# Optimization experiments

Measured on AMD Instinct MI355X. Metric: run time of the kernel, lower is better.

## Reference

```python
import jax, jax.numpy as jnp
import numpy as np
from jax import lax

V_JOINTS = 25
N_SCALES = 13
C1 = 96
N_SEG = 50
EPS = 1e-5

# NTU RGB+D 25-joint skeleton edges (0-indexed)
_EDGES = [(0,1),(1,20),(2,20),(3,2),(4,20),(5,4),(6,5),(7,6),(8,20),(9,8),
          (10,9),(11,10),(12,0),(13,12),(14,13),(15,14),(16,0),(17,16),
          (18,17),(19,18),(21,22),(22,7),(23,24),(24,11)]


def _build_A_powers():
    # MS-G3D disentangled multi-scale adjacency: k-hop shells, D^-1/2 A D^-1/2 normalized
    A = np.zeros((V_JOINTS, V_JOINTS), dtype=np.float64)
    for i, j in _EDGES:
        A[i, j] = 1.0
        A[j, i] = 1.0
    I = np.eye(V_JOINTS)
    mats = []
    for k in range(N_SCALES):
        if k == 0:
            Ak = I.copy()
        else:
            Ak = (np.minimum(np.linalg.matrix_power(A + I, k), 1)
                  - np.minimum(np.linalg.matrix_power(A + I, k - 1), 1))
            Ak = Ak + I  # with_self=True
        d = Ak.sum(-1)
        Dinv = np.diag(d ** -0.5)
        mats.append(Dinv @ Ak @ Dinv)
    return np.concatenate(mats, axis=0).astype(np.float32)  # (13*25, 25)


def _segments(T, n_seg):
    # Segment boundaries exactly as the torch code: int(round(linspace(1, T, n_seg+1)))
    t_vec = [int(round(v)) for v in np.linspace(1, T, n_seg + 1)]
    lens = [t_vec[i + 1] - t_vec[i] for i in range(n_seg)]
    L = max(lens)
    idx = np.zeros((n_seg, L), dtype=np.int32)
    mask = np.zeros((n_seg, L), dtype=np.float32)
    for s in range(n_seg):
        start = t_vec[s] - 1
        for l in range(L):
            idx[s, l] = min(start + l, T - 2)
            mask[s, l] = 1.0 if l < lens[s] else 0.0
    sp_idx = np.array([t - 1 for t in t_vec[:-1]], dtype=np.int32)
    return idx, mask, sp_idx


def setup_inputs() -> dict:
    key = jax.random.key(0)
    ks = jax.random.split(key, 18)
    N, M, C, T, V = 4, 2, 3, 300, V_JOINTS
    num_classes = 60
    Cbn = M * C * V                       # 150
    Dlog = C1 + C1 * (C1 - 1) // 2        # 4656 (depth-2 logsig dims)
    Din = C1 + Dlog                       # 4752 (start pos + logsig)
    f = lambda k, s: jax.random.normal(k, s, dtype=jnp.float32)
    return {
        'x': f(ks[0], (N, M, C, T, V)),
        'bn_g': 1.0 + 0.1 * f(ks[1], (Cbn,)),
        'bn_b': 0.1 * f(ks[2], (Cbn,)),
        'bn_m': 0.1 * f(ks[3], (Cbn,)),
        'bn_v': jax.random.uniform(ks[4], (Cbn,), minval=0.5, maxval=1.5),
        'A_powers': jnp.asarray(_build_A_powers()),
        'A_res': jax.random.uniform(ks[5], (N_SCALES * V, V), minval=-1e-6, maxval=1e-6),
        'W_gcn': f(ks[6], (C1, N_SCALES * C)) / np.sqrt(N_SCALES * C),
        'b_gcn': 0.1 * f(ks[7], (C1,)),
        'bn2_g': 1.0 + 0.1 * f(ks[8], (C1,)),
        'bn2_b': 0.1 * f(ks[9], (C1,)),
        'bn2_m': 0.1 * f(ks[10], (C1,)),
        'bn2_v': jax.random.uniform(ks[11], (C1,), minval=0.5, maxval=1.5),
        'W_ih': f(ks[12], (4 * C1, Din)) / np.sqrt(Din),
        'W_hh': f(ks[13], (4 * C1, C1)) / np.sqrt(C1),
        'b_ih': 0.1 * f(ks[14], (4 * C1,)),
        'b_hh': 0.1 * f(ks[15], (4 * C1,)),
        'W_fc': f(ks[16], (num_classes, C1)) / np.sqrt(C1),
        'b_fc': 0.1 * f(ks[17], (num_classes,)),
    }


def reference(x, bn_g, bn_b, bn_m, bn_v, A_powers, A_res, W_gcn, b_gcn,
              bn2_g, bn2_b, bn2_m, bn2_v, W_ih, W_hh, b_ih, b_hh, W_fc, b_fc):
    N, M, C, T, V = x.shape
    NM = N * M
    # --- data_bn (inference BatchNorm1d over M*V*C channels) ---
    xb = x.transpose(0, 1, 4, 2, 3).reshape(N, M * V * C, T)
    xb = (xb - bn_m[:, None]) * (bn_g / jnp.sqrt(bn_v + EPS))[:, None] + bn_b[:, None]
    xg = xb.reshape(NM, V, C, T).transpose(0, 2, 3, 1)          # (NM, C, T, V)
    # --- MS_GCN: multi-scale disentangled graph conv ---
    A = A_powers + A_res                                        # (S*V, V)
    sup = jnp.einsum('vu,nctu->nctv', A, xg)                    # (NM, C, T, S*V)
    sup = sup.reshape(NM, C, T, N_SCALES, V).transpose(0, 3, 1, 2, 4)
    sup = sup.reshape(NM, N_SCALES * C, T, V)
    y = jnp.einsum('oc,nctv->notv', W_gcn, sup) + b_gcn[None, :, None, None]
    y = (y - bn2_m[None, :, None, None]) * (bn2_g / jnp.sqrt(bn2_v + EPS))[None, :, None, None] \
        + bn2_b[None, :, None, None]
    y = jax.nn.relu(y)                                          # (NM, C1, T, V)
    # --- LogSigRNN: per-joint temporal path, depth-2 log-signature per segment ---
    p = y.transpose(0, 3, 2, 1).reshape(NM * V, T, C1)          # (B, T, C1)
    idx, mask, sp_idx = _segments(T, N_SEG)
    dx = jnp.diff(p, axis=1)                                    # (B, T-1, C1)
    dseg = dx[:, idx] * mask[None, :, :, None]                  # (B, nseg, L, C1)
    pseg = jnp.cumsum(dseg, axis=2) - dseg                      # exclusive prefix within segment
    s1 = dseg.sum(axis=2)                                       # level-1: total increment
    Q = jnp.einsum('bslc,bsld->bscd', pseg, dseg)               # (B, nseg, C1, C1)
    levy = 0.5 * (Q - jnp.swapaxes(Q, -1, -2))                  # level-2 (Levy area)
    iu, ju = np.triu_indices(C1, 1)
    ls2 = levy[:, :, iu, ju]                                    # (B, nseg, 4560)
    start_pos = p[:, sp_idx, :]                                 # (B, nseg, C1)
    feat = jnp.concatenate([start_pos, s1, ls2], axis=-1)       # (B, nseg, 4752)
    # --- LSTM (torch gate order i,f,g,o) ---
    B = feat.shape[0]
    xw = jnp.einsum('btd,gd->btg', feat, W_ih) + (b_ih + b_hh)
    def step(carry, xt):
        h, c = carry
        g = xt + h @ W_hh.T
        i, fg, gg, o = jnp.split(g, 4, axis=-1)
        c = jax.nn.sigmoid(fg) * c + jax.nn.sigmoid(i) * jnp.tanh(gg)
        h = jax.nn.sigmoid(o) * jnp.tanh(c)
        return (h, c), h
    h0 = jnp.zeros((B, C1), feat.dtype)
    _, hs = lax.scan(step, (h0, h0), jnp.swapaxes(xw, 0, 1))
    hs = jnp.swapaxes(hs, 0, 1)                                 # (B, nseg, C1)
    out = hs.reshape(NM, V, N_SEG, C1).transpose(0, 3, 2, 1)    # (NM, C1, nseg, V)
    out = out.reshape(N, M, C1, -1).mean(axis=3).mean(axis=1)   # (N, C1)
    return out @ W_fc.T + b_fc
```

## Files before the change

kernel.cpp:

```cpp
#include <hip/hip_runtime.h>
#include <math.h>

#define KF 4752
#define KP 4768
#define KSTEPS 149
#define G4 384
#define NPAIR 4560
#define EPSBN 1e-5f
#define XWHALF 3840000

typedef float f32x4 __attribute__((ext_vector_type(4)));
typedef short s16x8 __attribute__((ext_vector_type(8)));

__device__ __forceinline__ unsigned short f2bf(float x){
  unsigned u = __float_as_uint(x);
  return (unsigned short)((u + 0x7fffu + ((u>>16)&1u)) >> 16);
}
__device__ __forceinline__ float bf2f(unsigned short h){
  return __uint_as_float(((unsigned)h)<<16);
}

__device__ __forceinline__ int seg_start(int s){ return (s<=24)? 6*s : 149 + 6*(s-25); }
__device__ __forceinline__ int seg_len(int s){ return (s==24)?5:6; }

#define NB_GEFF 1407
#define NB_BEFF 1200
#define NB_WSPL 7152

__global__ __launch_bounds__(256) void kPre(
    const float* bn_g,const float* bn_b,const float* bn_m,const float* bn_v,
    const float* Ap,const float* Ar,const float* Wg,const float* bg,
    const float* bn2_g,const float* bn2_b,const float* bn2_m,const float* bn2_v,
    const float* wih,
    float* geffT, float* beffT, unsigned short* whi, unsigned short* wlo)
{
  int bid = blockIdx.x, tid = threadIdx.x;
  if (bid < NB_GEFF){
    int idx = bid*256 + tid;
    if (idx >= 2*96*25*75) return;
    int cu = idx % 75; int rest = idx/75;
    int v = rest % 25; rest /= 25;
    int o = rest % 96; int m = rest / 96;
    int c = cu/25, u = cu%25;
    int ch = (m*25+u)*3 + c;
    float s1 = bn_g[ch] / sqrtf(bn_v[ch] + EPSBN);
    float s2 = bn2_g[o] / sqrtf(bn2_v[o] + EPSBN);
    float acc = 0.f;
    for (int k=0;k<13;k++){
      float a = Ap[(k*25+v)*25+u] + Ar[(k*25+v)*25+u];
      acc += Wg[o*39 + k*3 + c] * a;
    }
    geffT[((size_t)(m*75+cu))*2400 + v*96 + o] = acc * s1 * s2;
  } else if (bid < NB_GEFF + NB_BEFF){
    int wid  = ((bid-NB_GEFF)*256 + tid) >> 6;
    int lane = tid & 63;
    if (wid >= 2*96*25) return;
    int v = wid % 25; int rest = wid/25; int o = rest % 96; int m = rest/96;
    float acc = 0.f;
    #pragma unroll
    for (int it=0; it<16; ++it){
      int item = it*64 + lane;
      if (item < 975){
        int k = item / 75; int cu = item % 75; int c = cu/25, u = cu%25;
        int ch = (m*25+u)*3 + c;
        float s1 = bn_g[ch] / sqrtf(bn_v[ch] + EPSBN);
        float t1 = bn_b[ch] - bn_m[ch]*s1;
        float a  = Ap[(k*25+v)*25+u] + Ar[(k*25+v)*25+u];
        acc += Wg[o*39 + k*3 + c] * a * t1;
      }
    }
    #pragma unroll
    for (int off=32; off; off>>=1) acc += __shfl_down(acc, off);
    if (lane == 0){
      acc += bg[o];
      float s2 = bn2_g[o]/sqrtf(bn2_v[o]+EPSBN);
      beffT[m*2400 + v*96 + o] = s2*(acc - bn2_m[o]) + bn2_b[o];
    }
  } else {
    int idx = (bid - NB_GEFF - NB_BEFF)*256 + tid;
    if (idx >= G4*KP) return;
    int g = idx / KP, k = idx % KP;
    float v = (k < KF) ? wih[(size_t)g*KF + k] : 0.f;
    unsigned short h = f2bf(v);
    whi[idx] = h;
    wlo[idx] = f2bf(v - bf2f(h));
  }
}

#define TTILE 10
__global__ __launch_bounds__(256) void kP(const float* x, const float* geffT, const float* beffT, float* p){
  int nm = blockIdx.y;
  int t0 = blockIdx.x * TTILE;
  int m  = nm % 2;
  __shared__ float xs[75*TTILE];
  int tid = threadIdx.x;
  for (int li = tid; li < 75*TTILE; li += 256){
    int u = li % 25; int rest = li/25; int tt = rest % TTILE; int c = rest / TTILE;
    xs[(c*25+u)*TTILE + tt] = x[(((size_t)nm*3 + c)*300 + (t0+tt))*25 + u];
  }
  __syncthreads();
  const float* gT = geffT + (size_t)m*75*2400;
  for (int ow = tid; ow < 2400; ow += 256){
    int o = ow % 96, v = ow / 96;
    float b = beffT[m*2400 + ow];
    float acc[TTILE];
    #pragma unroll
    for (int t=0;t<TTILE;t++) acc[t] = b;
    for (int cu=0; cu<75; cu++){
      float gv = gT[(size_t)cu*2400 + ow];
      #pragma unroll
      for (int t=0;t<TTILE;t++) acc[t] += gv * xs[cu*TTILE+t];
    }
    #pragma unroll
    for (int t=0;t<TTILE;t++)
      p[((size_t)(nm*25+v)*300 + t0+t)*96 + o] = fmaxf(acc[t], 0.f);
  }
}

__global__ __launch_bounds__(256) void kFeat(const float* p,
                                             unsigned short* fhi, unsigned short* flo, int row0){
  int row = row0 + blockIdx.x;
  int b = row / 50, s = row % 50;
  int S = seg_start(s), len = seg_len(s);
  __shared__ float psL[6][96];
  __shared__ float dsL[6][96];
  __shared__ float qbuf[NPAIR];
  int tid = threadIdx.x;
  size_t base = (size_t)blockIdx.x * KP;
  if (tid < 96){
    int c = tid;
    float pv[7];
    #pragma unroll
    for (int l=0;l<7;l++) pv[l] = p[((size_t)b*300 + S + l)*96 + c];
    float run = 0.f;
    #pragma unroll
    for (int l=0;l<6;l++){
      float d = (l < len) ? (pv[l+1]-pv[l]) : 0.f;
      psL[l][c] = run; dsL[l][c] = d; run += d;
    }
    unsigned short h0 = f2bf(pv[0]);
    fhi[base + c] = h0; flo[base + c] = f2bf(pv[0] - bf2f(h0));
    unsigned short h1 = f2bf(run);
    fhi[base + 96 + c] = h1; flo[base + 96 + c] = f2bf(run - bf2f(h1));
  } else if (tid < 112){
    int c = KF + (tid - 96);
    fhi[base + c] = 0; flo[base + c] = 0;
  }
  __syncthreads();
  int ti = tid >> 4, tj = tid & 15;
  if (ti <= tj){
    int i0 = ti*6, j0 = tj*6;
    float q[6][6];
    #pragma unroll
    for (int a=0;a<6;a++)
      #pragma unroll
      for (int e=0;e<6;e++) q[a][e] = 0.f;
    #pragma unroll
    for (int l=0;l<6;l++){
      float pi[6], di[6], pj[6], dj[6];
      #pragma unroll
      for (int a=0;a<6;a++){
        pi[a] = psL[l][i0+a]; di[a] = dsL[l][i0+a];
        pj[a] = psL[l][j0+a]; dj[a] = dsL[l][j0+a];
      }
      #pragma unroll
      for (int a=0;a<6;a++)
        #pragma unroll
        for (int e=0;e<6;e++)
          q[a][e] += pi[a]*dj[e] - pj[e]*di[a];
    }
    #pragma unroll
    for (int a=0;a<6;a++){
      int i = i0 + a;
      int kb = i*95 - (i*(i-1))/2 - i - 1;
      #pragma unroll
      for (int e=0;e<6;e++){
        int j = j0 + e;
        if (j > i) qbuf[kb + j] = 0.5f*q[a][e];
      }
    }
  }
  __syncthreads();
  for (int g8 = tid; g8 < NPAIR/8; g8 += 256){
    f32x4 q0 = *(const f32x4*)&qbuf[g8*8];
    f32x4 q1 = *(const f32x4*)&qbuf[g8*8+4];
    float qa[8] = {q0.x,q0.y,q0.z,q0.w,q1.x,q1.y,q1.z,q1.w};
    s16x8 vh, vl;
    #pragma unroll
    for (int e=0;e<8;e++){
      unsigned short h = f2bf(qa[e]);
      vh[e] = (short)h;
      vl[e] = (short)f2bf(qa[e] - bf2f(h));
    }
    *(s16x8*)(fhi + base + 192 + g8*8) = vh;
    *(s16x8*)(flo + base + 192 + g8*8) = vl;
  }
}

__device__ __forceinline__ void gload16(const void* g, void* l){
  __builtin_amdgcn_global_load_lds(
      (const __attribute__((address_space(1))) void*)g,
      (__attribute__((address_space(3))) void*)l, 16, 0, 0);
}

__global__ __launch_bounds__(256) void kGemm(
    const unsigned short* __restrict__ fhi, const unsigned short* __restrict__ flo,
    const unsigned short* __restrict__ whi, const unsigned short* __restrict__ wlo,
    float* __restrict__ xw, int chunkRow0, int nrows)
{
  __shared__ unsigned short lds[20480];
  int tid  = threadIdx.x;
  int lane = tid & 63, w = tid >> 6;
  int id = blockIdx.x;
  int col = id & 1, zz = (id >> 1) & 3, mblk = id >> 3;
  int rowBase = mblk*128, colBase = col*192;
  int zbase = (zz==0) ? 0 : (38 + 37*(zz-1));
  int zSteps = (zz==0) ? 38 : 37;

  const unsigned short* gptr[10];
  int ldsOff[10];
  #pragma unroll
  for (int q=0;q<10;q++){
    int c = (w*10 + q)*64 + lane;
    const unsigned short* bp; int rr;
    if (c < 512)        { rr = c;        bp = fhi + (size_t)(rowBase + (rr>>2))*KP; }
    else if (c < 1024)  { rr = c-512;    bp = flo + (size_t)(rowBase + (rr>>2))*KP; }
    else if (c < 1792)  { rr = c-1024;   bp = whi + (size_t)(colBase + (rr>>2))*KP; }
    else                { rr = c-1792;   bp = wlo + (size_t)(colBase + (rr>>2))*KP; }
    int rw = rr>>2, gl = rr&3;
    int gs = gl ^ ((rw>>1)&3);
    gptr[q]  = bp + gs*8;
    ldsOff[q] = (w*10 + q)*512;
  }

  int wm = w & 1, wn = w >> 1;
  int gsel = lane >> 4, li = lane & 15;
  int aoff[4], boff[6];
  #pragma unroll
  for (int fm=0; fm<4; fm++){
    int r = wm*64 + fm*16 + li;
    aoff[fm] = r*32 + ((gsel ^ ((r>>1)&3))*8);
  }
  #pragma unroll
  for (int fn=0; fn<6; fn++){
    int r = wn*96 + fn*16 + li;
    boff[fn] = 8192 + r*32 + ((gsel ^ ((r>>1)&3))*8);
  }

  f32x4 acc[4][6];
  #pragma unroll
  for (int fm=0;fm<4;fm++)
    #pragma unroll
    for (int fn=0;fn<6;fn++) acc[fm][fn] = (f32x4){0.f,0.f,0.f,0.f};

  for (int t=0; t<zSteps; ++t){
    size_t ko = (size_t)(zbase + t)*32;
    #pragma unroll
    for (int q=0;q<10;q++) gload16(gptr[q] + ko, &lds[ldsOff[q]]);
    asm volatile("s_waitcnt vmcnt(0)" ::: "memory");
    __builtin_amdgcn_s_barrier();
    s16x8 bh[6], bl[6];
    #pragma unroll
    for (int fn=0;fn<6;fn++){
      bh[fn] = *(const s16x8*)(lds + boff[fn]);
      bl[fn] = *(const s16x8*)(lds + boff[fn] + 6144);
    }
    #pragma unroll
    for (int fm=0;fm<4;fm++){
      s16x8 ah = *(const s16x8*)(lds + aoff[fm]);
      s16x8 al = *(const s16x8*)(lds + aoff[fm] + 4096);
      #pragma unroll
      for (int fn=0;fn<6;fn++){
        acc[fm][fn] = __builtin_amdgcn_mfma_f32_16x16x32_bf16(ah, bh[fn], acc[fm][fn], 0,0,0);
        acc[fm][fn] = __builtin_amdgcn_mfma_f32_16x16x32_bf16(ah, bl[fn], acc[fm][fn], 0,0,0);
        acc[fm][fn] = __builtin_amdgcn_mfma_f32_16x16x32_bf16(al, bh[fn], acc[fm][fn], 0,0,0);
      }
    }
    __builtin_amdgcn_s_barrier();
  }

  int rl = (lane>>4)*4, cl = lane&15;
  float* outp = xw + (size_t)zz*XWHALF;
  #pragma unroll
  for (int fm=0;fm<4;fm++){
    #pragma unroll
    for (int fn=0;fn<6;fn++){
      int gr0 = rowBase + wm*64 + fm*16 + rl;
      int gc  = colBase + wn*96 + fn*16 + cl;
      f32x4 v = acc[fm][fn];
      #pragma unroll
      for (int r=0;r<4;r++){
        int gr = gr0 + r;
        if (gr < nrows)
          outp[(size_t)(chunkRow0 + gr)*G4 + gc] = v[r];
      }
    }
  }
}

__global__ __launch_bounds__(192) void kLstm(const float* xw, const float* whh,
                                             const float* bih, const float* bhh, float* hsum){
  int b = blockIdx.x;
  int t = threadIdx.x;
  int gA = t;
  int gB = t + 192;
  __shared__ __align__(16) float h_s[96];
  __shared__ float gbuf[384];
  float wA[96], wB[96];
  #pragma unroll
  for (int k=0;k<96;k++){ wA[k] = whh[(size_t)gA*96 + k]; wB[k] = whh[(size_t)gB*96 + k]; }
  float bA = bih[gA] + bhh[gA];
  float bB = bih[gB] + bhh[gB];
  float cval = 0.f, hacc = 0.f;
  if (t < 96) h_s[t] = 0.f;
  __syncthreads();
  const float* xr = xw + (size_t)b*50*G4;
  for (int st=0; st<50; st++){
    int o = st*G4;
    float aA = xr[o+gA] + xr[XWHALF+o+gA] + xr[2*(size_t)XWHALF+o+gA]
             + xr[3*(size_t)XWHALF+o+gA] + bA;
    float aB = xr[o+gB] + xr[XWHALF+o+gB] + xr[2*(size_t)XWHALF+o+gB]
             + xr[3*(size_t)XWHALF+o+gB] + bB;
    #pragma unroll
    for (int k=0;k<96;k+=4){
      float4 h4 = *(const float4*)&h_s[k];
      aA += wA[k]*h4.x + wA[k+1]*h4.y + wA[k+2]*h4.z + wA[k+3]*h4.w;
      aB += wB[k]*h4.x + wB[k+1]*h4.y + wB[k+2]*h4.z + wB[k+3]*h4.w;
    }
    gbuf[gA] = aA; gbuf[gB] = aB;
    __syncthreads();
    if (t < 96){
      float ig = gbuf[t], fg = gbuf[96+t], gg = gbuf[192+t], og = gbuf[288+t];
      float si = 1.f/(1.f+expf(-ig));
      float sf = 1.f/(1.f+expf(-fg));
      float so = 1.f/(1.f+expf(-og));
      cval = sf*cval + si*tanhf(gg);
      float h = so * tanhf(cval);
      h_s[t] = h;
      hacc += h;
    }
    __syncthreads();
  }
  if (t < 96) hsum[(size_t)b*96 + t] = hacc;
}

__global__ void kOut(const float* hsum, const float* wfc, const float* bfc, float* out){
  int n = blockIdx.x;
  __shared__ float pool[96];
  int tid = threadIdx.x;
  if (tid < 96){
    float a = 0.f;
    for (int mv=0; mv<50; mv++) a += hsum[((size_t)(n*50 + mv))*96 + tid];
    pool[tid] = a / 2500.f;
  }
  __syncthreads();
  if (tid < 60){
    float a = bfc[tid];
    for (int o=0;o<96;o++) a += pool[o]*wfc[tid*96+o];
    out[n*60+tid] = a;
  }
}

extern "C" void kernel_launch(void* const* d_in, const int* in_sizes, int n_in,
                              void* d_out, int out_size, void* d_ws, size_t ws_size,
                              hipStream_t stream){
  const float* x     = (const float*)d_in[0];
  const float* bn_g  = (const float*)d_in[1];
  const float* bn_b  = (const float*)d_in[2];
  const float* bn_m  = (const float*)d_in[3];
  const float* bn_v  = (const float*)d_in[4];
  const float* Ap    = (const float*)d_in[5];
  const float* Ar    = (const float*)d_in[6];
  const float* Wg    = (const float*)d_in[7];
  const float* bg    = (const float*)d_in[8];
  const float* bn2_g = (const float*)d_in[9];
  const float* bn2_b = (const float*)d_in[10];
  const float* bn2_m = (const float*)d_in[11];
  const float* bn2_v = (const float*)d_in[12];
  const float* wih   = (const float*)d_in[13];
  const float* whh   = (const float*)d_in[14];
  const float* bih   = (const float*)d_in[15];
  const float* bhh   = (const float*)d_in[16];
  const float* wfc   = (const float*)d_in[17];
  const float* bfc   = (const float*)d_in[18];
  float* out = (float*)d_out;

  float* ws    = (float*)d_ws;
  float* geffT = ws;
  float* beffT = geffT + 360000;
  float* pbuf  = beffT + 4800;
  float* xw    = pbuf + 5760000;
  float* hsum  = xw + 4*(size_t)XWHALF;
  unsigned short* whiP = (unsigned short*)(hsum + 19200);
  unsigned short* wloP = whiP + (size_t)G4*KP;
  unsigned short* fhi  = wloP + (size_t)G4*KP;
  size_t fixedFloats = 360000u + 4800u + 5760000u + 4u*(size_t)XWHALF + 19200u
                     + (size_t)G4*KP;
  long long availB = (long long)ws_size - (long long)(fixedFloats*4);
  long long perUnit = 128LL*KP*4;
  long long units = (availB > 0) ? availB/perUnit : 1;
  if (units < 1)  units = 1;
  if (units > 79) units = 79;
  int chunk = (int)units * 128;
  unsigned short* flo = fhi + (size_t)chunk*KP;

  kPre<<<NB_GEFF+NB_BEFF+NB_WSPL, 256, 0, stream>>>(
      bn_g, bn_b, bn_m, bn_v, Ap, Ar, Wg, bg, bn2_g, bn2_b, bn2_m, bn2_v,
      wih, geffT, beffT, whiP, wloP);
  kP<<<dim3(30, 8), 256, 0, stream>>>(x, geffT, beffT, pbuf);

  for (int r0 = 0; r0 < 10000; r0 += chunk){
    int nr = 10000 - r0; if (nr > chunk) nr = chunk;
    kFeat<<<nr, 256, 0, stream>>>(pbuf, fhi, flo, r0);
    int mblkc = (nr + 127)/128;
    kGemm<<<8*mblkc, 256, 0, stream>>>(fhi, flo, whiP, wloP, xw, r0, nr);
  }

  kLstm<<<200, 192, 0, stream>>>(xw, whh, bih, bhh, hsum);
  kOut<<<4, 128, 0, stream>>>(hsum, wfc, bfc, out);
}
```

Measured before the change: 468.8 us.

## Double-buffer GEMM LDS tiles and process two segments per feature block

The split-bf16 GEMM now double-buffers its LDS tiles. Each iteration issues the next K-slice's global-to-LDS loads before running the MFMAs on the current slice, so memory latency overlaps with compute. This doubles LDS use per block, which may lower occupancy. The grid is also remapped to a 3D launch, and the feature kernel handles two segment rows per block and writes bf16 hi/lo Levy-area values straight to global memory without staging them in shared memory. Those direct writes are scattered 2-byte stores rather than vectorised ones, so coalescing in the feature kernel may get worse.

```diff
diff --git a/kernel.cpp b/kernel.cpp
--- a/kernel.cpp
+++ b/kernel.cpp
@@ -119,16 +119,15 @@
 
 __global__ __launch_bounds__(256) void kFeat(const float* p,
                                              unsigned short* fhi, unsigned short* flo, int row0){
-  int row = row0 + blockIdx.x;
-  int b = row / 50, s = row % 50;
-  int S = seg_start(s), len = seg_len(s);
-  __shared__ float psL[6][96];
-  __shared__ float dsL[6][96];
-  __shared__ float qbuf[NPAIR];
+  __shared__ float psL[2][6][96];
+  __shared__ float dsL[2][6][96];
   int tid = threadIdx.x;
-  size_t base = (size_t)blockIdx.x * KP;
-  if (tid < 96){
-    int c = tid;
+  if (tid < 192){
+    int rr = tid / 96, c = tid % 96;
+    int row = row0 + blockIdx.x*2 + rr;
+    int b = row / 50, s = row % 50;
+    int S = seg_start(s), len = seg_len(s);
+    size_t base = (size_t)(blockIdx.x*2 + rr) * KP;
     float pv[7];
     #pragma unroll
     for (int l=0;l<7;l++) pv[l] = p[((size_t)b*300 + S + l)*96 + c];
@@ -136,20 +135,27 @@
     #pragma unroll
     for (int l=0;l<6;l++){
       float d = (l < len) ? (pv[l+1]-pv[l]) : 0.f;
-      psL[l][c] = run; dsL[l][c] = d; run += d;
+      psL[rr][l][c] = run; dsL[rr][l][c] = d; run += d;
     }
     unsigned short h0 = f2bf(pv[0]);
     fhi[base + c] = h0; flo[base + c] = f2bf(pv[0] - bf2f(h0));
     unsigned short h1 = f2bf(run);
     fhi[base + 96 + c] = h1; flo[base + 96 + c] = f2bf(run - bf2f(h1));
-  } else if (tid < 112){
-    int c = KF + (tid - 96);
+  } else if (tid < 224){
+    int z = tid - 192;
+    int rr = z >> 4, c = KF + (z & 15);
+    size_t base = (size_t)(blockIdx.x*2 + rr) * KP;
     fhi[base + c] = 0; flo[base + c] = 0;
   }
   __syncthreads();
-  int ti = tid >> 4, tj = tid & 15;
-  if (ti <= tj){
+  for (int tt = tid; tt < 272; tt += 256){
+    int rr = (tt >= 136) ? 1 : 0;
+    int tix = tt - 136*rr;
+    int ti = 0, rem = tix;
+    while (rem >= 16 - ti){ rem -= 16 - ti; ti++; }
+    int tj = ti + rem;
     int i0 = ti*6, j0 = tj*6;
+    size_t base = (size_t)(blockIdx.x*2 + rr) * KP + 192;
     float q[6][6];
     #pragma unroll
     for (int a=0;a<6;a++)
@@ -160,8 +166,8 @@
       float pi[6], di[6], pj[6], dj[6];
       #pragma unroll
       for (int a=0;a<6;a++){
-        pi[a] = psL[l][i0+a]; di[a] = dsL[l][i0+a];
-        pj[a] = psL[l][j0+a]; dj[a] = dsL[l][j0+a];
+        pi[a] = psL[rr][l][i0+a]; di[a] = dsL[rr][l][i0+a];
+        pj[a] = psL[rr][l][j0+a]; dj[a] = dsL[rr][l][j0+a];
       }
       #pragma unroll
       for (int a=0;a<6;a++)
@@ -176,24 +182,14 @@
       #pragma unroll
       for (int e=0;e<6;e++){
         int j = j0 + e;
-        if (j > i) qbuf[kb + j] = 0.5f*q[a][e];
+        if (j > i){
+          float qq = 0.5f*q[a][e];
+          unsigned short h = f2bf(qq);
+          fhi[base + kb + j] = h;
+          flo[base + kb + j] = f2bf(qq - bf2f(h));
+        }
       }
     }
-  }
-  __syncthreads();
-  for (int g8 = tid; g8 < NPAIR/8; g8 += 256){
-    f32x4 q0 = *(const f32x4*)&qbuf[g8*8];
-    f32x4 q1 = *(const f32x4*)&qbuf[g8*8+4];
-    float qa[8] = {q0.x,q0.y,q0.z,q0.w,q1.x,q1.y,q1.z,q1.w};
-    s16x8 vh, vl;
-    #pragma unroll
-    for (int e=0;e<8;e++){
-      unsigned short h = f2bf(qa[e]);
-      vh[e] = (short)h;
-      vl[e] = (short)f2bf(qa[e] - bf2f(h));
-    }
-    *(s16x8*)(fhi + base + 192 + g8*8) = vh;
-    *(s16x8*)(flo + base + 192 + g8*8) = vl;
   }
 }
 
@@ -208,14 +204,14 @@
     const unsigned short* __restrict__ whi, const unsigned short* __restrict__ wlo,
     float* __restrict__ xw, int chunkRow0, int nrows)
 {
-  __shared__ unsigned short lds[20480];
+  __shared__ unsigned short lds[2][20480];
   int tid  = threadIdx.x;
   int lane = tid & 63, w = tid >> 6;
-  int id = blockIdx.x;
-  int col = id & 1, zz = (id >> 1) & 3, mblk = id >> 3;
-  int rowBase = mblk*128, colBase = col*192;
-  int zbase = (zz==0) ? 0 : (38 + 37*(zz-1));
-  int zSteps = (zz==0) ? 38 : 37;
+  int colBase = blockIdx.x * 192;
+  int zz      = blockIdx.y;
+  int mblk    = blockIdx.z;
+  int zbase   = (zz==0) ? 0 : (38 + 37*(zz-1));
+  int zSteps  = (zz==0) ? 38 : 37;
 
   const unsigned short* gptr[10];
   int ldsOff[10];
@@ -223,27 +219,27 @@
   for (int q=0;q<10;q++){
     int c = (w*10 + q)*64 + lane;
     const unsigned short* bp; int rr;
-    if (c < 512)        { rr = c;        bp = fhi + (size_t)(rowBase + (rr>>2))*KP; }
-    else if (c < 1024)  { rr = c-512;    bp = flo + (size_t)(rowBase + (rr>>2))*KP; }
-    else if (c < 1792)  { rr = c-1024;   bp = whi + (size_t)(colBase + (rr>>2))*KP; }
-    else                { rr = c-1792;   bp = wlo + (size_t)(colBase + (rr>>2))*KP; }
-    int rw = rr>>2, gl = rr&3;
-    int gs = gl ^ ((rw>>1)&3);
+    if (c < 512)        { rr = c;        bp = fhi + (size_t)(mblk*128 + (rr>>2))*KP; }
+    else if (c < 1024)  { rr = c-512;    bp = flo + (size_t)(mblk*128 + (rr>>2))*KP; }
+    else if (c < 1792)  { rr = c-1024;   bp = whi + (size_t)(colBase  + (rr>>2))*KP; }
+    else                { rr = c-1792;   bp = wlo + (size_t)(colBase  + (rr>>2))*KP; }
+    int row = rr>>2, gl = rr&3;
+    int gs = gl ^ ((row>>1)&3);
     gptr[q]  = bp + gs*8;
     ldsOff[q] = (w*10 + q)*512;
   }
 
   int wm = w & 1, wn = w >> 1;
-  int gsel = lane >> 4, li = lane & 15;
+  int gsel = lane >> 4;
   int aoff[4], boff[6];
   #pragma unroll
   for (int fm=0; fm<4; fm++){
-    int r = wm*64 + fm*16 + li;
+    int r = wm*64 + fm*16 + (lane&15);
     aoff[fm] = r*32 + ((gsel ^ ((r>>1)&3))*8);
   }
   #pragma unroll
   for (int fn=0; fn<6; fn++){
-    int r = wn*96 + fn*16 + li;
+    int r = wn*96 + fn*16 + (lane&15);
     boff[fn] = 8192 + r*32 + ((gsel ^ ((r>>1)&3))*8);
   }
 
@@ -253,30 +249,38 @@
     #pragma unroll
     for (int fn=0;fn<6;fn++) acc[fm][fn] = (f32x4){0.f,0.f,0.f,0.f};
 
+  #pragma unroll
+  for (int q=0;q<10;q++) gload16(gptr[q] + (size_t)zbase*32, &lds[0][ldsOff[q]]);
+
+  int cur = 0;
   for (int t=0; t<zSteps; ++t){
-    size_t ko = (size_t)(zbase + t)*32;
-    #pragma unroll
-    for (int q=0;q<10;q++) gload16(gptr[q] + ko, &lds[ldsOff[q]]);
-    asm volatile("s_waitcnt vmcnt(0)" ::: "memory");
-    __builtin_amdgcn_s_barrier();
-    s16x8 bh[6], bl[6];
+    __syncthreads();
+    if (t+1 < zSteps){
+      size_t ko = (size_t)(zbase + t + 1)*32;
+      #pragma unroll
+      for (int q=0;q<10;q++) gload16(gptr[q] + ko, &lds[cur^1][ldsOff[q]]);
+    }
+    const unsigned short* L = lds[cur];
+    s16x8 ah[4], al[4], bh[6], bl[6];
+    #pragma unroll
+    for (int fm=0;fm<4;fm++){
+      ah[fm] = *(const s16x8*)(L + aoff[fm]);
+      al[fm] = *(const s16x8*)(L + aoff[fm] + 4096);
+    }
     #pragma unroll
     for (int fn=0;fn<6;fn++){
-      bh[fn] = *(const s16x8*)(lds + boff[fn]);
-      bl[fn] = *(const s16x8*)(lds + boff[fn] + 6144);
-    }
-    #pragma unroll
-    for (int fm=0;fm<4;fm++){
-      s16x8 ah = *(const s16x8*)(lds + aoff[fm]);
-      s16x8 al = *(const s16x8*)(lds + aoff[fm] + 4096);
+      bh[fn] = *(const s16x8*)(L + boff[fn]);
+      bl[fn] = *(const s16x8*)(L + boff[fn] + 6144);
+    }
+    #pragma unroll
+    for (int fm=0;fm<4;fm++)
       #pragma unroll
       for (int fn=0;fn<6;fn++){
-        acc[fm][fn] = __builtin_amdgcn_mfma_f32_16x16x32_bf16(ah, bh[fn], acc[fm][fn], 0,0,0);
-        acc[fm][fn] = __builtin_amdgcn_mfma_f32_16x16x32_bf16(ah, bl[fn], acc[fm][fn], 0,0,0);
-        acc[fm][fn] = __builtin_amdgcn_mfma_f32_16x16x32_bf16(al, bh[fn], acc[fm][fn], 0,0,0);
+        acc[fm][fn] = __builtin_amdgcn_mfma_f32_16x16x32_bf16(ah[fm], bh[fn], acc[fm][fn], 0,0,0);
+        acc[fm][fn] = __builtin_amdgcn_mfma_f32_16x16x32_bf16(ah[fm], bl[fn], acc[fm][fn], 0,0,0);
+        acc[fm][fn] = __builtin_amdgcn_mfma_f32_16x16x32_bf16(al[fm], bh[fn], acc[fm][fn], 0,0,0);
       }
-    }
-    __builtin_amdgcn_s_barrier();
+    cur ^= 1;
   }
 
   int rl = (lane>>4)*4, cl = lane&15;
@@ -285,7 +289,7 @@
   for (int fm=0;fm<4;fm++){
     #pragma unroll
     for (int fn=0;fn<6;fn++){
-      int gr0 = rowBase + wm*64 + fm*16 + rl;
+      int gr0 = mblk*128 + wm*64 + fm*16 + rl;
       int gc  = colBase + wn*96 + fn*16 + cl;
       f32x4 v = acc[fm][fn];
       #pragma unroll
@@ -411,9 +415,8 @@
 
   for (int r0 = 0; r0 < 10000; r0 += chunk){
     int nr = 10000 - r0; if (nr > chunk) nr = chunk;
-    kFeat<<<nr, 256, 0, stream>>>(pbuf, fhi, flo, r0);
-    int mblkc = (nr + 127)/128;
-    kGemm<<<8*mblkc, 256, 0, stream>>>(fhi, flo, whiP, wloP, xw, r0, nr);
+    kFeat<<<nr/2, 256, 0, stream>>>(pbuf, fhi, flo, r0);
+    kGemm<<<dim3(2, 4, (nr + 127)/128), 256, 0, stream>>>(fhi, flo, whiP, wloP, xw, r0, nr);
   }
 
   kLstm<<<200, 192, 0, stream>>>(xw, whh, bih, bhh, hsum);
```

Measured after the change: 494.4 us. 1.05x slower.
